# Kernel optimization log

Hardware: AMD Instinct MI355X
Metric: run time of the kernel (lower is better)

The kernel has to match this reference:

```python
import jax, jax.numpy as jnp
import numpy as np

B, N, C, H, E, K = 2, 2048, 1024, 4096, 8, 2
TAU = 1.0


def setup_inputs() -> dict:
    key = jax.random.key(0)
    ks = jax.random.split(key, 9)
    x = jax.random.normal(ks[0], (B, N, C), dtype=jnp.float32)
    T = B * N
    u = jax.random.uniform(ks[1], (T, E), minval=1e-6, maxval=1.0 - 1e-6)
    gumbel_noise = -jnp.log(-jnp.log(u))  # Gumbel(0,1) samples
    s = 0.02
    gate_w = jax.random.normal(ks[2], (C, E), dtype=jnp.float32) * s
    gate_b = jnp.zeros((E,), dtype=jnp.float32)
    w1 = jax.random.normal(ks[3], (E, C, H), dtype=jnp.float32) * s
    b1 = jnp.zeros((E, H), dtype=jnp.float32)
    w2 = jax.random.normal(ks[4], (E, H, C), dtype=jnp.float32) * s
    b2 = jnp.zeros((E, C), dtype=jnp.float32)
    return {"x": x, "gumbel_noise": gumbel_noise, "gate_w": gate_w,
            "gate_b": gate_b, "w1": w1, "b1": b1, "w2": w2, "b2": b2}


def reference(x, gumbel_noise, gate_w, gate_b, w1, b1, w2, b2):
    Bb, Nn, Cc = x.shape
    x_flat = x.reshape(-1, Cc)                                  # [T, C]
    logits = x_flat @ gate_w + gate_b                           # [T, E]
    # F.gumbel_softmax(hard=False, tau=1): softmax((logits + g)/tau)
    gates = jax.nn.softmax((logits + gumbel_noise) / TAU, axis=-1)
    mean_gates = gates.mean(axis=0)
    load_balance_loss = jnp.sum(mean_gates * jnp.log(mean_gates + 1e-8))
    topk_vals, topk_idxs = jax.lax.top_k(gates, K)              # [T, K]
    T = x_flat.shape[0]
    # scatter top-k gate weights into a dense [T, E] combine matrix
    comb = jnp.zeros((T, E), dtype=gates.dtype)
    comb = comb.at[jnp.arange(T)[:, None], topk_idxs].set(topk_vals)
    # dense per-expert MLP over all tokens, then weighted combine
    h = jnp.einsum('tc,ech->teh', x_flat, w1) + b1              # [T, E, H]
    h = jax.nn.gelu(h, approximate=False)                        # exact GELU (nn.GELU)
    y = jnp.einsum('teh,ehc->tec', h, w2) + b2                  # [T, E, C]
    out = jnp.einsum('te,tec->tc', comb, y)                     # [T, C]
    return out.reshape(Bb, Nn, Cc), load_balance_loss
```

## Files before the change

### kernel.cpp

```cpp
#include <hip/hip_runtime.h>
#include <math.h>

#define TT  4096
#define CC  1024
#define HH  4096
#define EE  8
#define TKN 8192

typedef _Float16 f16x8 __attribute__((ext_vector_type(8)));
typedef float    f32x4 __attribute__((ext_vector_type(4)));

#define GLD_LDS16(g, l)                                                        \
    __builtin_amdgcn_global_load_lds(                                          \
        (const __attribute__((address_space(1))) void*)(g),                    \
        (__attribute__((address_space(3))) void*)(l), 16, 0, 0)

__global__ __launch_bounds__(256) void gate_kernel(
    const float* __restrict__ x, const float* __restrict__ gn,
    const float* __restrict__ gw, const float* __restrict__ gb,
    int* __restrict__ topk_idx, float* __restrict__ topk_w,
    int* __restrict__ counts, float* __restrict__ gsum)
{
    int wave = threadIdx.x >> 6, lane = threadIdx.x & 63;
    int t = blockIdx.x * 4 + wave;
    const float* xrow = x + (size_t)t * CC;

    double acc[EE];
#pragma unroll
    for (int e = 0; e < EE; e++) acc[e] = 0.0;

#pragma unroll
    for (int i = 0; i < CC / 64; i++) {
        int c = i * 64 + lane;
        float xv = xrow[c];
        const float4* g4 = reinterpret_cast<const float4*>(gw + (size_t)c * EE);
        float4 g0 = g4[0], g1 = g4[1];
        double xd = (double)xv;
        acc[0] += xd * (double)g0.x; acc[1] += xd * (double)g0.y;
        acc[2] += xd * (double)g0.z; acc[3] += xd * (double)g0.w;
        acc[4] += xd * (double)g1.x; acc[5] += xd * (double)g1.y;
        acc[6] += xd * (double)g1.z; acc[7] += xd * (double)g1.w;
    }
#pragma unroll
    for (int e = 0; e < EE; e++)
#pragma unroll
        for (int off = 32; off > 0; off >>= 1)
            acc[e] += __shfl_xor(acc[e], off);

    double z[EE], m = -1e300;
#pragma unroll
    for (int e = 0; e < EE; e++) {
        z[e] = acc[e] + (double)gb[e] + (double)gn[(size_t)t * EE + e];
        m = fmax(m, z[e]);
    }
    double p[EE], s = 0.0;
#pragma unroll
    for (int e = 0; e < EE; e++) { p[e] = exp(z[e] - m); s += p[e]; }
    double inv = 1.0 / s;
    double g[EE];
#pragma unroll
    for (int e = 0; e < EE; e++) g[e] = p[e] * inv;

    int i1 = 0; double v1 = g[0];
#pragma unroll
    for (int e = 1; e < EE; e++) if (g[e] > v1) { v1 = g[e]; i1 = e; }
    int i2 = -1; double v2 = -1.0;
#pragma unroll
    for (int e = 0; e < EE; e++) if (e != i1 && g[e] > v2) { v2 = g[e]; i2 = e; }

    if (lane == 0) {
        topk_idx[t * 2 + 0] = i1; topk_w[t * 2 + 0] = (float)v1;
        topk_idx[t * 2 + 1] = i2; topk_w[t * 2 + 1] = (float)v2;
        atomicAdd(&counts[i1], 1);
        atomicAdd(&counts[i2], 1);
    }

    __shared__ float gp[4][EE];
    if (lane == 0) {
#pragma unroll
        for (int e = 0; e < EE; e++) gp[wave][e] = (float)g[e];
    }
    __syncthreads();
    if (threadIdx.x < EE) {
        float s4 = gp[0][threadIdx.x] + gp[1][threadIdx.x] +
                   gp[2][threadIdx.x] + gp[3][threadIdx.x];
        atomicAdd(&gsum[threadIdx.x], s4);
    }
}

__global__ __launch_bounds__(256) void transpose_f16_kernel(
    const float* __restrict__ src, _Float16* __restrict__ dst, int R, int Ccols)
{
    __shared__ float tile[64][65];
    int e = blockIdx.z;
    const float* s = src + (size_t)e * R * Ccols;
    _Float16* d = dst + (size_t)e * R * Ccols;
    int c0 = blockIdx.x * 64, r0 = blockIdx.y * 64;
    int tid = threadIdx.x;

    int lr = tid >> 4;
    int lc = (tid & 15) * 4;
#pragma unroll
    for (int i = 0; i < 4; i++) {
        int r = lr + i * 16;
        float4 v = *reinterpret_cast<const float4*>(
            s + (size_t)(r0 + r) * Ccols + c0 + lc);
        tile[r][lc + 0] = v.x; tile[r][lc + 1] = v.y;
        tile[r][lc + 2] = v.z; tile[r][lc + 3] = v.w;
    }
    __syncthreads();

    int oc = tid >> 2;
    int orr = (tid & 3) * 16;
    f16x8 o0, o1;
#pragma unroll
    for (int j = 0; j < 8; j++) o0[j] = (_Float16)tile[orr + j][oc];
#pragma unroll
    for (int j = 0; j < 8; j++) o1[j] = (_Float16)tile[orr + 8 + j][oc];
    *reinterpret_cast<f16x8*>(d + (size_t)(c0 + oc) * R + r0 + orr)     = o0;
    *reinterpret_cast<f16x8*>(d + (size_t)(c0 + oc) * R + r0 + orr + 8) = o1;
}

__global__ void scan_kernel(const int* __restrict__ counts, int* __restrict__ offsets,
                            const float* __restrict__ gsum, float* __restrict__ loss_out)
{
    if (threadIdx.x == 0) {
        int o = 0;
#pragma unroll
        for (int e = 0; e < EE; e++) { offsets[e] = o; o += counts[e]; }
        offsets[EE] = o;
        float L = 0.f;
#pragma unroll
        for (int e = 0; e < EE; e++) {
            float me = gsum[e] / (float)TT;
            L += me * logf(me + 1e-8f);
        }
        *loss_out = L;
    }
}

__global__ __launch_bounds__(256) void scatter_kernel(
    const int* __restrict__ topk_idx, const int* __restrict__ offsets,
    int* __restrict__ fill, int* __restrict__ rowtok, int* __restrict__ posmap)
{
    int t = blockIdx.x * 256 + threadIdx.x;
#pragma unroll
    for (int k = 0; k < 2; k++) {
        int e = topk_idx[t * 2 + k];
        int pos = offsets[e] + atomicAdd(&fill[e], 1);
        rowtok[pos] = t;
        posmap[t * 2 + k] = pos;
    }
}

__global__ __launch_bounds__(256) void gather_kernel(
    const float* __restrict__ x, const int* __restrict__ rowtok,
    _Float16* __restrict__ xg)
{
    int p = blockIdx.x * 2 + (threadIdx.x >> 7);
    int c = (threadIdx.x & 127) * 8;
    int t = rowtok[p];
    const float4* s = reinterpret_cast<const float4*>(x + (size_t)t * CC + c);
    float4 v0 = s[0], v1 = s[1];
    f16x8 o;
    o[0] = (_Float16)v0.x; o[1] = (_Float16)v0.y;
    o[2] = (_Float16)v0.z; o[3] = (_Float16)v0.w;
    o[4] = (_Float16)v1.x; o[5] = (_Float16)v1.y;
    o[6] = (_Float16)v1.z; o[7] = (_Float16)v1.w;
    *reinterpret_cast<f16x8*>(xg + (size_t)p * CC + c) = o;
}

__global__ __launch_bounds__(256) void gemm1_kernel(
    const _Float16* __restrict__ xg, const _Float16* __restrict__ w1t,
    const float* __restrict__ b1, const int* __restrict__ offsets,
    _Float16* __restrict__ h)
{
    int GX = gridDim.x, GY = gridDim.y;
    int nwg = GX * GY * (int)gridDim.z;
    int f = blockIdx.x + GX * (blockIdx.y + GY * blockIdx.z);
    int cpx = nwg >> 3;
    f = (f & 7) * cpx + (f >> 3);
    int bx = f % GX; int tq = f / GX; int by = tq % GY; int bz = tq / GY;

    int e = bz;
    int segs = offsets[e];
    int M = offsets[e + 1] - segs;
    int m0 = bx * 128;
    if (m0 >= M) return;
    int n0 = by * 128;

    __shared__ __align__(16) _Float16 As[2][128][64];
    __shared__ __align__(16) _Float16 Bs[2][128][64];

    int tid = threadIdx.x;
    int wave = tid >> 6, lane = tid & 63;
    int wm = (wave >> 1) * 64, wn = (wave & 1) * 64;
    int lrow = lane & 15, kg = lane >> 4;

    const _Float16* wB = w1t + (size_t)e * HH * CC;

    const _Float16* ap[4]; const _Float16* bp[4];
    int lofs[4];
#pragma unroll
    for (int j = 0; j < 4; j++) {
        int ch = (wave * 4 + j) * 64 + lane;
        int row = ch >> 3, kc = ch & 7;
        int rm = m0 + row; if (rm >= M) rm = M - 1;
        ap[j] = xg + (size_t)(segs + rm) * CC + kc * 8;
        bp[j] = wB + (size_t)(n0 + row) * CC + kc * 8;
        lofs[j] = ch * 8;
    }

    f32x4 acc[4][4];
#pragma unroll
    for (int i = 0; i < 4; i++)
#pragma unroll
        for (int j = 0; j < 4; j++)
#pragma unroll
            for (int r = 0; r < 4; r++) acc[i][j][r] = 0.f;

    _Float16* A0 = &As[0][0][0];
    _Float16* B0 = &Bs[0][0][0];

#pragma unroll
    for (int j = 0; j < 4; j++) {
        GLD_LDS16(ap[j], A0 + lofs[j]);
        GLD_LDS16(bp[j], B0 + lofs[j]);
        ap[j] += 64; bp[j] += 64;
    }
    __syncthreads();

    int cur = 0;
    const int NIT = CC / 64;
    for (int it = 0; it < NIT; ++it) {
        if (it + 1 < NIT) {
            _Float16* ad = A0 + (cur ^ 1) * (128 * 64);
            _Float16* bd = B0 + (cur ^ 1) * (128 * 64);
#pragma unroll
            for (int j = 0; j < 4; j++) {
                GLD_LDS16(ap[j], ad + lofs[j]);
                GLD_LDS16(bp[j], bd + lofs[j]);
                ap[j] += 64; bp[j] += 64;
            }
        }
        const _Float16* Ac = A0 + cur * (128 * 64);
        const _Float16* Bc = B0 + cur * (128 * 64);
        f16x8 aF[2][4], bF[2][4];
#pragma unroll
        for (int s = 0; s < 2; s++)
#pragma unroll
            for (int i = 0; i < 4; i++) {
                aF[s][i] = *reinterpret_cast<const f16x8*>(
                    Ac + (wm + i * 16 + lrow) * 64 + s * 32 + kg * 8);
                bF[s][i] = *reinterpret_cast<const f16x8*>(
                    Bc + (wn + i * 16 + lrow) * 64 + s * 32 + kg * 8);
            }
#pragma unroll
        for (int s = 0; s < 2; s++)
#pragma unroll
            for (int mi = 0; mi < 4; mi++)
#pragma unroll
                for (int ni = 0; ni < 4; ni++)
                    acc[mi][ni] = __builtin_amdgcn_mfma_f32_16x16x32_f16(
                        aF[s][mi], bF[s][ni], acc[mi][ni], 0, 0, 0);
        __syncthreads();
        cur ^= 1;
    }

    int rbase = (lane >> 4) * 4;
#pragma unroll
    for (int mi = 0; mi < 4; mi++) {
#pragma unroll
        for (int ni = 0; ni < 4; ni++) {
            int gcol = n0 + wn + ni * 16 + lrow;
            float bias = b1[(size_t)e * HH + gcol];
#pragma unroll
            for (int r = 0; r < 4; r++) {
                int rowl = m0 + wm + mi * 16 + rbase + r;
                if (rowl < M) {
                    float v = acc[mi][ni][r] + bias;
                    v = 0.5f * v * (1.0f + erff(v * 0.70710678118654752f));
                    h[(size_t)(segs + rowl) * HH + gcol] = (_Float16)v;
                }
            }
        }
    }
}

__global__ __launch_bounds__(256) void gemm2_kernel(
    const _Float16* __restrict__ h, const _Float16* __restrict__ w2t,
    const float* __restrict__ b2, const int* __restrict__ offsets,
    float* __restrict__ y)
{
    int GX = gridDim.x, GY = gridDim.y;
    int nwg = GX * GY * (int)gridDim.z;
    int f = blockIdx.x + GX * (blockIdx.y + GY * blockIdx.z);
    int cpx = nwg >> 3;
    f = (f & 7) * cpx + (f >> 3);
    int bx = f % GX; int tq = f / GX; int by = tq % GY; int bz = tq / GY;

    int e = bz;
    int segs = offsets[e];
    int M = offsets[e + 1] - segs;
    int m0 = bx * 128;
    if (m0 >= M) return;
    int n0 = by * 128;

    __shared__ __align__(16) _Float16 As[2][128][64];
    __shared__ __align__(16) _Float16 Bs[2][128][64];

    int tid = threadIdx.x;
    int wave = tid >> 6, lane = tid & 63;
    int wm = (wave >> 1) * 64, wn = (wave & 1) * 64;
    int lrow = lane & 15, kg = lane >> 4;

    const _Float16* wB = w2t + (size_t)e * CC * HH;

    const _Float16* ap[4]; const _Float16* bp[4];
    int lofs[4];
#pragma unroll
    for (int j = 0; j < 4; j++) {
        int ch = (wave * 4 + j) * 64 + lane;
        int row = ch >> 3, kc = ch & 7;
        int rm = m0 + row; if (rm >= M) rm = M - 1;
        ap[j] = h  + (size_t)(segs + rm) * HH + kc * 8;
        bp[j] = wB + (size_t)(n0 + row) * HH + kc * 8;
        lofs[j] = ch * 8;
    }

    f32x4 acc[4][4];
#pragma unroll
    for (int i = 0; i < 4; i++)
#pragma unroll
        for (int j = 0; j < 4; j++)
#pragma unroll
            for (int r = 0; r < 4; r++) acc[i][j][r] = 0.f;

    _Float16* A0 = &As[0][0][0];
    _Float16* B0 = &Bs[0][0][0];

#pragma unroll
    for (int j = 0; j < 4; j++) {
        GLD_LDS16(ap[j], A0 + lofs[j]);
        GLD_LDS16(bp[j], B0 + lofs[j]);
        ap[j] += 64; bp[j] += 64;
    }
    __syncthreads();

    int cur = 0;
    const int NIT = HH / 64;
    for (int it = 0; it < NIT; ++it) {
        if (it + 1 < NIT) {
            _Float16* ad = A0 + (cur ^ 1) * (128 * 64);
            _Float16* bd = B0 + (cur ^ 1) * (128 * 64);
#pragma unroll
            for (int j = 0; j < 4; j++) {
                GLD_LDS16(ap[j], ad + lofs[j]);
                GLD_LDS16(bp[j], bd + lofs[j]);
                ap[j] += 64; bp[j] += 64;
            }
        }
        const _Float16* Ac = A0 + cur * (128 * 64);
        const _Float16* Bc = B0 + cur * (128 * 64);
        f16x8 aF[2][4], bF[2][4];
#pragma unroll
        for (int s = 0; s < 2; s++)
#pragma unroll
            for (int i = 0; i < 4; i++) {
                aF[s][i] = *reinterpret_cast<const f16x8*>(
                    Ac + (wm + i * 16 + lrow) * 64 + s * 32 + kg * 8);
                bF[s][i] = *reinterpret_cast<const f16x8*>(
                    Bc + (wn + i * 16 + lrow) * 64 + s * 32 + kg * 8);
            }
#pragma unroll
        for (int s = 0; s < 2; s++)
#pragma unroll
            for (int mi = 0; mi < 4; mi++)
#pragma unroll
                for (int ni = 0; ni < 4; ni++)
                    acc[mi][ni] = __builtin_amdgcn_mfma_f32_16x16x32_f16(
                        aF[s][mi], bF[s][ni], acc[mi][ni], 0, 0, 0);
        __syncthreads();
        cur ^= 1;
    }

    int rbase = (lane >> 4) * 4;
#pragma unroll
    for (int mi = 0; mi < 4; mi++) {
#pragma unroll
        for (int ni = 0; ni < 4; ni++) {
            int gcol = n0 + wn + ni * 16 + lrow;
            float bias = b2[(size_t)e * CC + gcol];
#pragma unroll
            for (int r = 0; r < 4; r++) {
                int rowl = m0 + wm + mi * 16 + rbase + r;
                if (rowl < M)
                    y[(size_t)(segs + rowl) * CC + gcol] = acc[mi][ni][r] + bias;
            }
        }
    }
}

__global__ __launch_bounds__(256) void combine_kernel(
    const float* __restrict__ y, const int* __restrict__ posmap,
    const float* __restrict__ topk_w, float* __restrict__ out)
{
    int t = blockIdx.x * 2 + (threadIdx.x >> 7);
    int c = (threadIdx.x & 127) * 8;
    int p0 = posmap[t * 2 + 0], p1 = posmap[t * 2 + 1];
    float wa = topk_w[t * 2 + 0], wb = topk_w[t * 2 + 1];
    const float4* a = reinterpret_cast<const float4*>(y + (size_t)p0 * CC + c);
    const float4* b = reinterpret_cast<const float4*>(y + (size_t)p1 * CC + c);
    float4 a0 = a[0], a1 = a[1], b0 = b[0], b1 = b[1];
    float4 r0, r1;
    r0.x = wa * a0.x + wb * b0.x; r0.y = wa * a0.y + wb * b0.y;
    r0.z = wa * a0.z + wb * b0.z; r0.w = wa * a0.w + wb * b0.w;
    r1.x = wa * a1.x + wb * b1.x; r1.y = wa * a1.y + wb * b1.y;
    r1.z = wa * a1.z + wb * b1.z; r1.w = wa * a1.w + wb * b1.w;
    float4* o = reinterpret_cast<float4*>(out + (size_t)t * CC + c);
    o[0] = r0; o[1] = r1;
}

extern "C" void kernel_launch(void* const* d_in, const int* in_sizes, int n_in,
                              void* d_out, int out_size, void* d_ws, size_t ws_size,
                              hipStream_t stream)
{
    const float* x  = (const float*)d_in[0];
    const float* gn = (const float*)d_in[1];
    const float* gw = (const float*)d_in[2];
    const float* gb = (const float*)d_in[3];
    const float* w1 = (const float*)d_in[4];
    const float* b1 = (const float*)d_in[5];
    const float* w2 = (const float*)d_in[6];
    const float* b2 = (const float*)d_in[7];
    float* out = (float*)d_out;

    char* w = (char*)d_ws;
    int*   counts  = (int*)(w + 0);
    int*   fill    = (int*)(w + 32);
    int*   offsets = (int*)(w + 64);
    float* gsum    = (float*)(w + 128);
    size_t off = 256;
    int*   topk_idx = (int*)(w + off);   off += (size_t)TT * 2 * 4;
    float* topk_w   = (float*)(w + off); off += (size_t)TT * 2 * 4;
    int*   rowtok   = (int*)(w + off);   off += (size_t)TKN * 4;
    int*   posmap   = (int*)(w + off);   off += (size_t)TKN * 4;
    _Float16* xg  = (_Float16*)(w + off); off += (size_t)TKN * CC * 2;
    _Float16* w1t = (_Float16*)(w + off); off += (size_t)EE * HH * CC * 2;
    _Float16* w2t = (_Float16*)(w + off); off += (size_t)EE * CC * HH * 2;
    _Float16* hbuf = (_Float16*)(w + off); off += (size_t)TKN * HH * 2;
    float* ybuf = (float*)w1t;

    (void)hipMemsetAsync(d_ws, 0, 256, stream);

    gate_kernel<<<TT / 4, 256, 0, stream>>>(x, gn, gw, gb, topk_idx, topk_w,
                                            counts, gsum);
    transpose_f16_kernel<<<dim3(HH / 64, CC / 64, EE), 256, 0, stream>>>(
        w1, w1t, CC, HH);
    transpose_f16_kernel<<<dim3(CC / 64, HH / 64, EE), 256, 0, stream>>>(
        w2, w2t, HH, CC);
    scan_kernel<<<1, 64, 0, stream>>>(counts, offsets, gsum, out + (size_t)TT * CC);
    scatter_kernel<<<TT / 256, 256, 0, stream>>>(topk_idx, offsets, fill,
                                                 rowtok, posmap);
    gather_kernel<<<TKN / 2, 256, 0, stream>>>(x, rowtok, xg);
    gemm1_kernel<<<dim3(12, HH / 128, EE), 256, 0, stream>>>(xg, w1t, b1,
                                                             offsets, hbuf);
    gemm2_kernel<<<dim3(12, CC / 128, EE), 256, 0, stream>>>(
        hbuf, w2t, b2, offsets, ybuf);
    combine_kernel<<<TT / 2, 256, 0, stream>>>(ybuf, posmap, topk_w, out);
}
```

Measured before the change: 1.002 ms.

## Use 256x256 tiles, 4-stage LDS pipeline, and split-K for expert GEMMs

```diff
diff --git a/kernel.cpp b/kernel.cpp
--- a/kernel.cpp
+++ b/kernel.cpp
@@ -14,6 +14,12 @@
     __builtin_amdgcn_global_load_lds(                                          \
         (const __attribute__((address_space(1))) void*)(g),                    \
         (__attribute__((address_space(3))) void*)(l), 16, 0, 0)
+
+#define BOUNDARY(N)                                                            \
+    do {                                                                       \
+        asm volatile("s_waitcnt vmcnt(" #N ")" ::: "memory");                  \
+        __builtin_amdgcn_s_barrier();                                          \
+    } while (0)
 
 __global__ __launch_bounds__(256) void gate_kernel(
     const float* __restrict__ x, const float* __restrict__ gn,
@@ -170,7 +176,7 @@
     *reinterpret_cast<f16x8*>(xg + (size_t)p * CC + c) = o;
 }
 
-__global__ __launch_bounds__(256) void gemm1_kernel(
+__global__ __launch_bounds__(512, 2) void gemm1_kernel(
     const _Float16* __restrict__ xg, const _Float16* __restrict__ w1t,
     const float* __restrict__ b1, const int* __restrict__ offsets,
     _Float16* __restrict__ h)
@@ -185,91 +191,97 @@
     int e = bz;
     int segs = offsets[e];
     int M = offsets[e + 1] - segs;
-    int m0 = bx * 128;
+    int m0 = bx * 256;
     if (m0 >= M) return;
-    int n0 = by * 128;
-
-    __shared__ __align__(16) _Float16 As[2][128][64];
-    __shared__ __align__(16) _Float16 Bs[2][128][64];
+    int n0 = by * 256;
+
+    __shared__ __align__(16) _Float16 As[4][256 * 32];
+    __shared__ __align__(16) _Float16 Bs[4][256 * 32];
+    _Float16* AsF = &As[0][0];
+    _Float16* BsF = &Bs[0][0];
 
     int tid = threadIdx.x;
     int wave = tid >> 6, lane = tid & 63;
-    int wm = (wave >> 1) * 64, wn = (wave & 1) * 64;
+    int wm = (wave >> 2) * 128, wn = (wave & 3) * 64;
     int lrow = lane & 15, kg = lane >> 4;
+    int aoff = (wm + lrow) * 32 + kg * 8;
+    int boff = (wn + lrow) * 32 + kg * 8;
 
     const _Float16* wB = w1t + (size_t)e * HH * CC;
 
-    const _Float16* ap[4]; const _Float16* bp[4];
-    int lofs[4];
-#pragma unroll
-    for (int j = 0; j < 4; j++) {
-        int ch = (wave * 4 + j) * 64 + lane;
-        int row = ch >> 3, kc = ch & 7;
-        int rm = m0 + row; if (rm >= M) rm = M - 1;
-        ap[j] = xg + (size_t)(segs + rm) * CC + kc * 8;
-        bp[j] = wB + (size_t)(n0 + row) * CC + kc * 8;
-        lofs[j] = ch * 8;
-    }
-
-    f32x4 acc[4][4];
-#pragma unroll
-    for (int i = 0; i < 4; i++)
+    int r0c = tid >> 2, cc = tid & 3;
+    int rmA0 = m0 + r0c;       if (rmA0 >= M) rmA0 = M - 1;
+    int rmA1 = m0 + 128 + r0c; if (rmA1 >= M) rmA1 = M - 1;
+    const _Float16* ap0 = xg + (size_t)(segs + rmA0) * CC + cc * 8;
+    const _Float16* ap1 = xg + (size_t)(segs + rmA1) * CC + cc * 8;
+    const _Float16* bp0 = wB + (size_t)(n0 + r0c) * CC + cc * 8;
+    const _Float16* bp1 = wB + (size_t)(n0 + 128 + r0c) * CC + cc * 8;
+    int c0 = tid * 8;
+
+    f32x4 acc[8][4];
+#pragma unroll
+    for (int i = 0; i < 8; i++)
 #pragma unroll
         for (int j = 0; j < 4; j++)
 #pragma unroll
             for (int r = 0; r < 4; r++) acc[i][j][r] = 0.f;
 
-    _Float16* A0 = &As[0][0][0];
-    _Float16* B0 = &Bs[0][0][0];
-
-#pragma unroll
-    for (int j = 0; j < 4; j++) {
-        GLD_LDS16(ap[j], A0 + lofs[j]);
-        GLD_LDS16(bp[j], B0 + lofs[j]);
-        ap[j] += 64; bp[j] += 64;
-    }
-    __syncthreads();
-
-    int cur = 0;
-    const int NIT = CC / 64;
-    for (int it = 0; it < NIT; ++it) {
-        if (it + 1 < NIT) {
-            _Float16* ad = A0 + (cur ^ 1) * (128 * 64);
-            _Float16* bd = B0 + (cur ^ 1) * (128 * 64);
-#pragma unroll
-            for (int j = 0; j < 4; j++) {
-                GLD_LDS16(ap[j], ad + lofs[j]);
-                GLD_LDS16(bp[j], bd + lofs[j]);
-                ap[j] += 64; bp[j] += 64;
-            }
-        }
-        const _Float16* Ac = A0 + cur * (128 * 64);
-        const _Float16* Bc = B0 + cur * (128 * 64);
-        f16x8 aF[2][4], bF[2][4];
-#pragma unroll
-        for (int s = 0; s < 2; s++)
-#pragma unroll
-            for (int i = 0; i < 4; i++) {
-                aF[s][i] = *reinterpret_cast<const f16x8*>(
-                    Ac + (wm + i * 16 + lrow) * 64 + s * 32 + kg * 8);
-                bF[s][i] = *reinterpret_cast<const f16x8*>(
-                    Bc + (wn + i * 16 + lrow) * 64 + s * 32 + kg * 8);
-            }
-#pragma unroll
-        for (int s = 0; s < 2; s++)
-#pragma unroll
-            for (int mi = 0; mi < 4; mi++)
-#pragma unroll
-                for (int ni = 0; ni < 4; ni++)
-                    acc[mi][ni] = __builtin_amdgcn_mfma_f32_16x16x32_f16(
-                        aF[s][mi], bF[s][ni], acc[mi][ni], 0, 0, 0);
-        __syncthreads();
-        cur ^= 1;
-    }
+    auto STAGE = [&](int nb) {
+        _Float16* ad = AsF + nb * (256 * 32);
+        _Float16* bd = BsF + nb * (256 * 32);
+        GLD_LDS16(ap0, ad + c0);
+        GLD_LDS16(ap1, ad + 4096 + c0);
+        GLD_LDS16(bp0, bd + c0);
+        GLD_LDS16(bp1, bd + 4096 + c0);
+        ap0 += 32; ap1 += 32; bp0 += 32; bp1 += 32;
+    };
+
+    auto TILE = [&](int t, bool stage) {
+        const _Float16* Ab = AsF + (t & 3) * (256 * 32) + aoff;
+        const _Float16* Bb = BsF + (t & 3) * (256 * 32) + boff;
+        if (stage) STAGE((t + 3) & 3);
+        f16x8 aF[4], bF[4];
+#pragma unroll
+        for (int j = 0; j < 4; j++)
+            bF[j] = *reinterpret_cast<const f16x8*>(Bb + j * 512);
+#pragma unroll
+        for (int i = 0; i < 4; i++)
+            aF[i] = *reinterpret_cast<const f16x8*>(Ab + i * 512);
+        __builtin_amdgcn_s_setprio(1);
+#pragma unroll
+        for (int i = 0; i < 4; i++)
+#pragma unroll
+            for (int j = 0; j < 4; j++)
+                acc[i][j] = __builtin_amdgcn_mfma_f32_16x16x32_f16(
+                    aF[i], bF[j], acc[i][j], 0, 0, 0);
+        __builtin_amdgcn_s_setprio(0);
+#pragma unroll
+        for (int i = 0; i < 4; i++)
+            aF[i] = *reinterpret_cast<const f16x8*>(Ab + (4 + i) * 512);
+        __builtin_amdgcn_s_setprio(1);
+#pragma unroll
+        for (int i = 0; i < 4; i++)
+#pragma unroll
+            for (int j = 0; j < 4; j++)
+                acc[4 + i][j] = __builtin_amdgcn_mfma_f32_16x16x32_f16(
+                    aF[i], bF[j], acc[4 + i][j], 0, 0, 0);
+        __builtin_amdgcn_s_setprio(0);
+    };
+
+    const int NK = CC / 32;
+    STAGE(0); STAGE(1); STAGE(2);
+    BOUNDARY(8);
+    for (int t = 0; t <= NK - 4; ++t) {
+        TILE(t, true);
+        BOUNDARY(8);
+    }
+    TILE(NK - 3, false); BOUNDARY(4);
+    TILE(NK - 2, false); BOUNDARY(0);
+    TILE(NK - 1, false);
 
     int rbase = (lane >> 4) * 4;
 #pragma unroll
-    for (int mi = 0; mi < 4; mi++) {
+    for (int mi = 0; mi < 8; mi++) {
 #pragma unroll
         for (int ni = 0; ni < 4; ni++) {
             int gcol = n0 + wn + ni * 16 + lrow;
@@ -287,7 +299,7 @@
     }
 }
 
-__global__ __launch_bounds__(256) void gemm2_kernel(
+__global__ __launch_bounds__(512, 2) void gemm2_kernel(
     const _Float16* __restrict__ h, const _Float16* __restrict__ w2t,
     const float* __restrict__ b2, const int* __restrict__ offsets,
     float* __restrict__ y)
@@ -302,100 +314,109 @@
     int e = bz;
     int segs = offsets[e];
     int M = offsets[e + 1] - segs;
-    int m0 = bx * 128;
+    int m0 = bx * 256;
     if (m0 >= M) return;
-    int n0 = by * 128;
-
-    __shared__ __align__(16) _Float16 As[2][128][64];
-    __shared__ __align__(16) _Float16 Bs[2][128][64];
+    int kz = by >> 2;
+    int n0 = (by & 3) * 256;
+    int kbeg = kz * (HH / 2);
+
+    __shared__ __align__(16) _Float16 As[4][256 * 32];
+    __shared__ __align__(16) _Float16 Bs[4][256 * 32];
+    _Float16* AsF = &As[0][0];
+    _Float16* BsF = &Bs[0][0];
 
     int tid = threadIdx.x;
     int wave = tid >> 6, lane = tid & 63;
-    int wm = (wave >> 1) * 64, wn = (wave & 1) * 64;
+    int wm = (wave >> 2) * 128, wn = (wave & 3) * 64;
     int lrow = lane & 15, kg = lane >> 4;
+    int aoff = (wm + lrow) * 32 + kg * 8;
+    int boff = (wn + lrow) * 32 + kg * 8;
 
     const _Float16* wB = w2t + (size_t)e * CC * HH;
 
-    const _Float16* ap[4]; const _Float16* bp[4];
-    int lofs[4];
-#pragma unroll
-    for (int j = 0; j < 4; j++) {
-        int ch = (wave * 4 + j) * 64 + lane;
-        int row = ch >> 3, kc = ch & 7;
-        int rm = m0 + row; if (rm >= M) rm = M - 1;
-        ap[j] = h  + (size_t)(segs + rm) * HH + kc * 8;
-        bp[j] = wB + (size_t)(n0 + row) * HH + kc * 8;
-        lofs[j] = ch * 8;
-    }
-
-    f32x4 acc[4][4];
-#pragma unroll
-    for (int i = 0; i < 4; i++)
+    int r0c = tid >> 2, cc = tid & 3;
+    int rmA0 = m0 + r0c;       if (rmA0 >= M) rmA0 = M - 1;
+    int rmA1 = m0 + 128 + r0c; if (rmA1 >= M) rmA1 = M - 1;
+    const _Float16* ap0 = h + (size_t)(segs + rmA0) * HH + kbeg + cc * 8;
+    const _Float16* ap1 = h + (size_t)(segs + rmA1) * HH + kbeg + cc * 8;
+    const _Float16* bp0 = wB + (size_t)(n0 + r0c) * HH + kbeg + cc * 8;
+    const _Float16* bp1 = wB + (size_t)(n0 + 128 + r0c) * HH + kbeg + cc * 8;
+    int c0 = tid * 8;
+
+    f32x4 acc[8][4];
+#pragma unroll
+    for (int i = 0; i < 8; i++)
 #pragma unroll
         for (int j = 0; j < 4; j++)
 #pragma unroll
             for (int r = 0; r < 4; r++) acc[i][j][r] = 0.f;
 
-    _Float16* A0 = &As[0][0][0];
-    _Float16* B0 = &Bs[0][0][0];
-
-#pragma unroll
-    for (int j = 0; j < 4; j++) {
-        GLD_LDS16(ap[j], A0 + lofs[j]);
-        GLD_LDS16(bp[j], B0 + lofs[j]);
-        ap[j] += 64; bp[j] += 64;
-    }
-    __syncthreads();
-
-    int cur = 0;
-    const int NIT = HH / 64;
-    for (int it = 0; it < NIT; ++it) {
-        if (it + 1 < NIT) {
-            _Float16* ad = A0 + (cur ^ 1) * (128 * 64);
-            _Float16* bd = B0 + (cur ^ 1) * (128 * 64);
-#pragma unroll
-            for (int j = 0; j < 4; j++) {
-                GLD_LDS16(ap[j], ad + lofs[j]);
-                GLD_LDS16(bp[j], bd + lofs[j]);
-                ap[j] += 64; bp[j] += 64;
-            }
-        }
-        const _Float16* Ac = A0 + cur * (128 * 64);
-        const _Float16* Bc = B0 + cur * (128 * 64);
-        f16x8 aF[2][4], bF[2][4];
-#pragma unroll
-        for (int s = 0; s < 2; s++)
-#pragma unroll
-            for (int i = 0; i < 4; i++) {
-                aF[s][i] = *reinterpret_cast<const f16x8*>(
-                    Ac + (wm + i * 16 + lrow) * 64 + s * 32 + kg * 8);
-                bF[s][i] = *reinterpret_cast<const f16x8*>(
-                    Bc + (wn + i * 16 + lrow) * 64 + s * 32 + kg * 8);
-            }
-#pragma unroll
-        for (int s = 0; s < 2; s++)
-#pragma unroll
-            for (int mi = 0; mi < 4; mi++)
-#pragma unroll
-                for (int ni = 0; ni < 4; ni++)
-                    acc[mi][ni] = __builtin_amdgcn_mfma_f32_16x16x32_f16(
-                        aF[s][mi], bF[s][ni], acc[mi][ni], 0, 0, 0);
-        __syncthreads();
-        cur ^= 1;
-    }
-
+    auto STAGE = [&](int nb) {
+        _Float16* ad = AsF + nb * (256 * 32);
+        _Float16* bd = BsF + nb * (256 * 32);
+        GLD_LDS16(ap0, ad + c0);
+        GLD_LDS16(ap1, ad + 4096 + c0);
+        GLD_LDS16(bp0, bd + c0);
+        GLD_LDS16(bp1, bd + 4096 + c0);
+        ap0 += 32; ap1 += 32; bp0 += 32; bp1 += 32;
+    };
+
+    auto TILE = [&](int t, bool stage) {
+        const _Float16* Ab = AsF + (t & 3) * (256 * 32) + aoff;
+        const _Float16* Bb = BsF + (t & 3) * (256 * 32) + boff;
+        if (stage) STAGE((t + 3) & 3);
+        f16x8 aF[4], bF[4];
+#pragma unroll
+        for (int j = 0; j < 4; j++)
+            bF[j] = *reinterpret_cast<const f16x8*>(Bb + j * 512);
+#pragma unroll
+        for (int i = 0; i < 4; i++)
+            aF[i] = *reinterpret_cast<const f16x8*>(Ab + i * 512);
+        __builtin_amdgcn_s_setprio(1);
+#pragma unroll
+        for (int i = 0; i < 4; i++)
+#pragma unroll
+            for (int j = 0; j < 4; j++)
+                acc[i][j] = __builtin_amdgcn_mfma_f32_16x16x32_f16(
+                    aF[i], bF[j], acc[i][j], 0, 0, 0);
+        __builtin_amdgcn_s_setprio(0);
+#pragma unroll
+        for (int i = 0; i < 4; i++)
+            aF[i] = *reinterpret_cast<const f16x8*>(Ab + (4 + i) * 512);
+        __builtin_amdgcn_s_setprio(1);
+#pragma unroll
+        for (int i = 0; i < 4; i++)
+#pragma unroll
+            for (int j = 0; j < 4; j++)
+                acc[4 + i][j] = __builtin_amdgcn_mfma_f32_16x16x32_f16(
+                    aF[i], bF[j], acc[4 + i][j], 0, 0, 0);
+        __builtin_amdgcn_s_setprio(0);
+    };
+
+    const int NK = (HH / 2) / 32;
+    STAGE(0); STAGE(1); STAGE(2);
+    BOUNDARY(8);
+    for (int t = 0; t <= NK - 4; ++t) {
+        TILE(t, true);
+        BOUNDARY(8);
+    }
+    TILE(NK - 3, false); BOUNDARY(4);
+    TILE(NK - 2, false); BOUNDARY(0);
+    TILE(NK - 1, false);
+
+    float* yk = y + (size_t)kz * TKN * CC;
     int rbase = (lane >> 4) * 4;
 #pragma unroll
-    for (int mi = 0; mi < 4; mi++) {
+    for (int mi = 0; mi < 8; mi++) {
 #pragma unroll
         for (int ni = 0; ni < 4; ni++) {
             int gcol = n0 + wn + ni * 16 + lrow;
-            float bias = b2[(size_t)e * CC + gcol];
+            float bias = (kz == 0) ? b2[(size_t)e * CC + gcol] : 0.f;
 #pragma unroll
             for (int r = 0; r < 4; r++) {
                 int rowl = m0 + wm + mi * 16 + rbase + r;
                 if (rowl < M)
-                    y[(size_t)(segs + rowl) * CC + gcol] = acc[mi][ni][r] + bias;
+                    yk[(size_t)(segs + rowl) * CC + gcol] = acc[mi][ni][r] + bias;
             }
         }
     }
@@ -409,14 +430,22 @@
     int c = (threadIdx.x & 127) * 8;
     int p0 = posmap[t * 2 + 0], p1 = posmap[t * 2 + 1];
     float wa = topk_w[t * 2 + 0], wb = topk_w[t * 2 + 1];
-    const float4* a = reinterpret_cast<const float4*>(y + (size_t)p0 * CC + c);
-    const float4* b = reinterpret_cast<const float4*>(y + (size_t)p1 * CC + c);
-    float4 a0 = a[0], a1 = a[1], b0 = b[0], b1 = b[1];
+    const float* y1 = y + (size_t)TKN * CC;
+    const float4* a0 = reinterpret_cast<const float4*>(y  + (size_t)p0 * CC + c);
+    const float4* a1 = reinterpret_cast<const float4*>(y1 + (size_t)p0 * CC + c);
+    const float4* b0 = reinterpret_cast<const float4*>(y  + (size_t)p1 * CC + c);
+    const float4* b1 = reinterpret_cast<const float4*>(y1 + (size_t)p1 * CC + c);
     float4 r0, r1;
-    r0.x = wa * a0.x + wb * b0.x; r0.y = wa * a0.y + wb * b0.y;
-    r0.z = wa * a0.z + wb * b0.z; r0.w = wa * a0.w + wb * b0.w;
-    r1.x = wa * a1.x + wb * b1.x; r1.y = wa * a1.y + wb * b1.y;
-    r1.z = wa * a1.z + wb * b1.z; r1.w = wa * a1.w + wb * b1.w;
+    float4 av0 = a0[0], av1 = a0[1], aw0 = a1[0], aw1 = a1[1];
+    float4 bv0 = b0[0], bv1 = b0[1], bw0 = b1[0], bw1 = b1[1];
+    r0.x = wa * (av0.x + aw0.x) + wb * (bv0.x + bw0.x);
+    r0.y = wa * (av0.y + aw0.y) + wb * (bv0.y + bw0.y);
+    r0.z = wa * (av0.z + aw0.z) + wb * (bv0.z + bw0.z);
+    r0.w = wa * (av0.w + aw0.w) + wb * (bv0.w + bw0.w);
+    r1.x = wa * (av1.x + aw1.x) + wb * (bv1.x + bw1.x);
+    r1.y = wa * (av1.y + aw1.y) + wb * (bv1.y + bw1.y);
+    r1.z = wa * (av1.z + aw1.z) + wb * (bv1.z + bw1.z);
+    r1.w = wa * (av1.w + aw1.w) + wb * (bv1.w + bw1.w);
     float4* o = reinterpret_cast<float4*>(out + (size_t)t * CC + c);
     o[0] = r0; o[1] = r1;
 }
@@ -463,9 +492,9 @@
     scatter_kernel<<<TT / 256, 256, 0, stream>>>(topk_idx, offsets, fill,
                                                  rowtok, posmap);
     gather_kernel<<<TKN / 2, 256, 0, stream>>>(x, rowtok, xg);
-    gemm1_kernel<<<dim3(12, HH / 128, EE), 256, 0, stream>>>(xg, w1t, b1,
-                                                             offsets, hbuf);
-    gemm2_kernel<<<dim3(12, CC / 128, EE), 256, 0, stream>>>(
+    gemm1_kernel<<<dim3(6, HH / 256, EE), 512, 0, stream>>>(xg, w1t, b1,
+                                                            offsets, hbuf);
+    gemm2_kernel<<<dim3(6, 2 * (CC / 256), EE), 512, 0, stream>>>(
         hbuf, w2t, b2, offsets, ybuf);
     combine_kernel<<<TT / 2, 256, 0, stream>>>(ybuf, posmap, topk_w, out);
 }
```

After: 876.3 us. 1.14x faster.
